# Optimization experiments

Measured on AMD Instinct MI355X. Metric: run time of the kernel, lower is better.

The kernel has to match this reference:

```python
import jax, jax.numpy as jnp
import numpy as np

B, S, H = 16, 2048, 768
MAX_NUM = 400     # max relation pairs per sample (ragged, masked)
LABELS = 97
MID = 768


def setup_inputs() -> dict:
    key = jax.random.key(0)
    k1, k2, k3, k4, k5 = jax.random.split(key, 5)
    outs = jax.random.normal(k1, (B, S, H), dtype=jnp.float32)
    rels = jax.random.randint(k2, (B, MAX_NUM), 0, LABELS)
    start = jnp.ones((B,), dtype=jnp.int32)                     # markers start at pos 1
    num = jax.random.randint(k3, (B,), 1, MAX_NUM + 1)          # ragged counts in [1, MAX_NUM]
    rels_pos = jnp.stack([start, num], axis=1)                  # [B, 2]
    W1 = jax.random.normal(k4, (2 * H, MID), dtype=jnp.float32) * (1.0 / np.sqrt(2 * H))
    b1 = jnp.zeros((MID,), dtype=jnp.float32)
    W2 = jax.random.normal(k5, (MID, LABELS), dtype=jnp.float32) * (1.0 / np.sqrt(MID))
    b2 = jnp.zeros((LABELS,), dtype=jnp.float32)
    return {"outs": outs, "rels": rels, "rels_pos": rels_pos,
            "W1": W1, "b1": b1, "W2": W2, "b2": b2}


def reference(outs, rels, rels_pos, W1, b1, W2, b2):
    # outs: [B, S, H] encoder hidden states; rels_pos[:, 0]=start, [:, 1]=num (ragged)
    start = rels_pos[:, 0]          # [B]
    num = rels_pos[:, 1]            # [B]
    i = jnp.arange(MAX_NUM)         # [N]
    mask = i[None, :] < num[:, None]                 # [B, N] valid-pair mask
    pos1 = start[:, None] + 4 * i[None, :]           # head marker positions
    pos2 = pos1 + 2                                  # tail marker positions
    pos1 = jnp.clip(pos1, 0, S - 1)
    pos2 = jnp.clip(pos2, 0, S - 1)
    v1 = jnp.take_along_axis(outs, pos1[:, :, None], axis=1)   # [B, N, H]
    v2 = jnp.take_along_axis(outs, pos2[:, :, None], axis=1)   # [B, N, H]
    marker_vec = jnp.concatenate([v1, v2], axis=-1)             # [B, N, 2H]
    h = jax.nn.relu(jnp.einsum('bnd,dm->bnm', marker_vec, W1) + b1)
    logits = jnp.einsum('bnm,ml->bnl', h, W2) + b2              # [B, N, L]
    logp = jax.nn.log_softmax(logits, axis=-1)
    nll = -jnp.take_along_axis(logp, rels[:, :, None], axis=-1)[..., 0]  # [B, N]
    maskf = mask.astype(logits.dtype)
    loss = jnp.sum(nll * maskf) / jnp.sum(maskf)                # mean CE over valid pairs
    pred = jnp.where(mask, jnp.argmax(logits, axis=-1), -1)     # [B, N], -1 = padding
    label_vec = jnp.where(mask, rels, -1)
    return loss, pred, label_vec
```

## Files before the change

### kernel.cpp

```cpp
#include <hip/hip_runtime.h>
#include <hip/hip_bf16.h>
#include <math.h>

#define BB   16
#define SS   2048
#define HH   768
#define MAXN 400
#define LBL  97
#define MIDD 768
#define KTOT 1536

#define K2_XTILES 25
#define W1S_JOBS  (192 * 768)

typedef __attribute__((ext_vector_type(8)))  __bf16 bf16x8;
typedef __attribute__((ext_vector_type(16))) float  f32x16;

__global__ __launch_bounds__(256)
void k0_split(const float* __restrict__ W1, ushort* __restrict__ hi,
              ushort* __restrict__ lo)
{
    const int job = blockIdx.x * 256 + threadIdx.x;
    if (job >= W1S_JOBS) return;
    const int g   = job / 768;
    const int col = job - g * 768;
    bf16x8 hv, lv;
    #pragma unroll
    for (int j = 0; j < 8; ++j) {
        const float f = W1[(size_t)(g * 8 + j) * MIDD + col];
        const __bf16 hb = (__bf16)f;
        hv[j] = hb;
        lv[j] = (__bf16)(f - (float)hb);
    }
    ((bf16x8*)hi)[job] = hv;
    ((bf16x8*)lo)[job] = lv;
}

__global__ __launch_bounds__(256, 4)
void k1_gemm1(const float* __restrict__ outs, const int* __restrict__ rels_pos,
              const ushort* __restrict__ w1hi, const ushort* __restrict__ w1lo,
              const float* __restrict__ b1, float* __restrict__ h)
{
    const int b  = blockIdx.z;
    const int n0 = blockIdx.x * 128;
    const int i0 = blockIdx.y * 64;
    const int num = rels_pos[2 * b + 1];
    if (i0 >= num) return;
    const int start = rels_pos[2 * b + 0];

    __shared__ __bf16 Ah[4][64][8];
    __shared__ __bf16 Al[4][64][8];
    __shared__ __bf16 Bh[4][128][8];
    __shared__ __bf16 Bl[4][128][8];

    const int tid = threadIdx.x;

    const int srow = tid & 63;
    const int sg   = tid >> 6;
    const int irow = i0 + srow;
    int p1 = start + 4 * irow;     p1 = min(max(p1, 0), SS - 1);
    int p2 = start + 4 * irow + 2; p2 = min(max(p2, 0), SS - 1);
    const float* arow1 = outs + (size_t)(b * SS + p1) * HH;
    const float* arow2 = outs + (size_t)(b * SS + p2) * HH;

    const int bc  = tid & 127;
    const int bg1 = tid >> 7;
    const int bg2 = 2 + (tid >> 7);
    const bf16x8* WH = (const bf16x8*)w1hi;
    const bf16x8* WL = (const bf16x8*)w1lo;

    const int lane = tid & 63;
    const int wid  = tid >> 6;
    const int wr   = wid >> 1;
    const int wc   = wid & 1;
    const int l31  = lane & 31;
    const int lhi  = lane >> 5;

    f32x16 acc[2];
    #pragma unroll
    for (int n = 0; n < 2; ++n)
        #pragma unroll
        for (int j = 0; j < 16; ++j) acc[n][j] = 0.f;

    float4 aU, aV;
    bf16x8 pB0, pB1, pB2, pB3;
    {
        const int k = sg * 8;
        const float* s = arow1 + k;
        aU = *(const float4*)(s);
        aV = *(const float4*)(s + 4);
        const size_t i1 = (size_t)bg1 * 768 + n0 + bc;
        const size_t i2 = (size_t)bg2 * 768 + n0 + bc;
        pB0 = WH[i1]; pB1 = WL[i1]; pB2 = WH[i2]; pB3 = WL[i2];
    }

    for (int kt = 0; kt < KTOT / 32; ++kt) {
        {
            const float fa[8] = {aU.x, aU.y, aU.z, aU.w, aV.x, aV.y, aV.z, aV.w};
            bf16x8 ah, al;
            #pragma unroll
            for (int j = 0; j < 8; ++j) {
                const __bf16 hb = (__bf16)fa[j];
                ah[j] = hb;
                al[j] = (__bf16)(fa[j] - (float)hb);
            }
            *(bf16x8*)&Ah[sg][srow][0] = ah;
            *(bf16x8*)&Al[sg][srow][0] = al;
            *(bf16x8*)&Bh[bg1][bc][0]  = pB0;
            *(bf16x8*)&Bl[bg1][bc][0]  = pB1;
            *(bf16x8*)&Bh[bg2][bc][0]  = pB2;
            *(bf16x8*)&Bl[bg2][bc][0]  = pB3;
        }
        __syncthreads();

        if (kt + 1 < KTOT / 32) {
            const int k0 = (kt + 1) * 32;
            const int k  = k0 + sg * 8;
            const float* s = (k < HH) ? (arow1 + k) : (arow2 + (k - HH));
            aU = *(const float4*)(s);
            aV = *(const float4*)(s + 4);
            const size_t base = (size_t)(k0 >> 3) * 768 + n0 + bc;
            const size_t i1 = base + (size_t)bg1 * 768;
            const size_t i2 = base + (size_t)bg2 * 768;
            pB0 = WH[i1]; pB1 = WL[i1]; pB2 = WH[i2]; pB3 = WL[i2];
        }

        #pragma unroll
        for (int s = 0; s < 2; ++s) {
            const int kg   = 2 * s + lhi;
            const int arow = wr * 32 + l31;
            const bf16x8 xh = *(const bf16x8*)&Ah[kg][arow][0];
            const bf16x8 xl = *(const bf16x8*)&Al[kg][arow][0];
            #pragma unroll
            for (int n = 0; n < 2; ++n) {
                const int bcol = wc * 64 + n * 32 + l31;
                const bf16x8 yh = *(const bf16x8*)&Bh[kg][bcol][0];
                const bf16x8 yl = *(const bf16x8*)&Bl[kg][bcol][0];
                acc[n] = __builtin_amdgcn_mfma_f32_32x32x16_bf16(xh, yh, acc[n], 0, 0, 0);
                acc[n] = __builtin_amdgcn_mfma_f32_32x32x16_bf16(xh, yl, acc[n], 0, 0, 0);
                acc[n] = __builtin_amdgcn_mfma_f32_32x32x16_bf16(xl, yh, acc[n], 0, 0, 0);
            }
        }
        __syncthreads();
    }

    #pragma unroll
    for (int n = 0; n < 2; ++n) {
        const int colg = n0 + wc * 64 + n * 32 + l31;
        const float bv = b1[colg];
        #pragma unroll
        for (int j = 0; j < 16; ++j) {
            const int row = (j & 3) + 8 * (j >> 2) + 4 * lhi;
            const int i = i0 + wr * 32 + row;
            if (i < MAXN)
                h[((size_t)b * MAXN + i) * MIDD + colg] = fmaxf(acc[n][j] + bv, 0.f);
        }
    }
}

__global__ __launch_bounds__(256, 2)
void k2_head(const float* __restrict__ h, const int* __restrict__ rels,
             const int* __restrict__ rels_pos,
             const float* __restrict__ W2, const float* __restrict__ b2,
             float* __restrict__ out, float* __restrict__ partials)
{
    const int b   = blockIdx.y;
    const int i0  = blockIdx.x * 16;
    const int num = rels_pos[2 * b + 1];
    const int tid = threadIdx.x;
    const int blk = blockIdx.y * gridDim.x + blockIdx.x;

    if (tid < 16) {
        const int i = i0 + tid;
        if (i < MAXN && i >= num) {
            out[1 + b * MAXN + i] = -1.0f;
            out[1 + BB * MAXN + b * MAXN + i] = -1.0f;
        }
    }
    if (i0 >= num) { if (tid == 0) partials[blk] = 0.f; return; }

    __shared__ __align__(16) float hs[MIDD][16];
    __shared__ float wave_nll[4];

    {
        const int row = tid & 15;
        const int kc0 = (tid >> 4) * 4;
        const int hrow_i = min(i0 + row, MAXN - 1);
        const float* hrow = h + ((size_t)b * MAXN + hrow_i) * MIDD;
        #pragma unroll
        for (int j = 0; j < 12; ++j) {
            const int k = kc0 + j * 64;
            const float4 v = *(const float4*)(hrow + k);
            hs[k + 0][row] = v.x;
            hs[k + 1][row] = v.y;
            hs[k + 2][row] = v.z;
            hs[k + 3][row] = v.w;
        }
    }
    __syncthreads();

    const int lane = tid & 63;
    const int wv   = tid >> 6;
    const int c    = lane;
    const bool has2 = (lane + 64) < LBL;
    const int c2   = has2 ? (lane + 64) : (LBL - 1);

    float acc0[4], acc1[4];
    #pragma unroll
    for (int r = 0; r < 4; ++r) { acc0[r] = 0.f; acc1[r] = 0.f; }

    float wA[8], wB[8], nAr[8], nBr[8];
    #pragma unroll
    for (int j = 0; j < 8; ++j) {
        wA[j] = W2[(size_t)j * LBL + c];
        wB[j] = W2[(size_t)j * LBL + c2];
    }
    for (int kbase = 0; kbase < MIDD; kbase += 8) {
        const bool more = (kbase + 8) < MIDD;
        if (more) {
            #pragma unroll
            for (int j = 0; j < 8; ++j) {
                nAr[j] = W2[(size_t)(kbase + 8 + j) * LBL + c];
                nBr[j] = W2[(size_t)(kbase + 8 + j) * LBL + c2];
            }
        }
        #pragma unroll
        for (int j = 0; j < 8; ++j) {
            const float4 hv = *(const float4*)&hs[kbase + j][wv * 4];
            acc0[0] += hv.x * wA[j]; acc0[1] += hv.y * wA[j];
            acc0[2] += hv.z * wA[j]; acc0[3] += hv.w * wA[j];
            acc1[0] += hv.x * wB[j]; acc1[1] += hv.y * wB[j];
            acc1[2] += hv.z * wB[j]; acc1[3] += hv.w * wB[j];
        }
        if (more) {
            #pragma unroll
            for (int j = 0; j < 8; ++j) { wA[j] = nAr[j]; wB[j] = nBr[j]; }
        }
    }
    const float bc  = b2[c];
    const float bc2 = b2[c2];
    #pragma unroll
    for (int r = 0; r < 4; ++r) { acc0[r] += bc; acc1[r] += bc2; }

    float nll_acc = 0.f;
    #pragma unroll
    for (int r = 0; r < 4; ++r) {
        const int i = i0 + wv * 4 + r;
        if (i >= num || i >= MAXN) continue;
        const float v1 = acc0[r];
        const float v2 = has2 ? acc1[r] : -INFINITY;
        float bv = v1; int bi = c;
        if (v2 > v1) { bv = v2; bi = lane + 64; }
        #pragma unroll
        for (int off = 32; off > 0; off >>= 1) {
            const float ov = __shfl_xor(bv, off);
            const int   oi = __shfl_xor(bi, off);
            if (ov > bv || (ov == bv && oi < bi)) { bv = ov; bi = oi; }
        }
        float se = expf(v1 - bv) + (has2 ? expf(v2 - bv) : 0.f);
        #pragma unroll
        for (int off = 32; off > 0; off >>= 1) se += __shfl_xor(se, off);
        const int lbl = rels[b * MAXN + i];
        float tv = (c == lbl ? v1 : 0.f) + ((has2 && (lane + 64) == lbl) ? v2 : 0.f);
        #pragma unroll
        for (int off = 32; off > 0; off >>= 1) tv += __shfl_xor(tv, off);
        const float nll = bv + logf(se) - tv;
        if (lane == 0) {
            nll_acc += nll;
            out[1 + b * MAXN + i] = (float)bi;
            out[1 + BB * MAXN + b * MAXN + i] = (float)lbl;
        }
    }
    if (lane == 0) wave_nll[wv] = nll_acc;
    __syncthreads();
    if (tid == 0)
        partials[blk] = wave_nll[0] + wave_nll[1] + wave_nll[2] + wave_nll[3];
}

__global__ void k3_final(const float* __restrict__ partials,
                         const int* __restrict__ rels_pos, float* __restrict__ out)
{
    const int lane = threadIdx.x;
    float v = 0.f;
    for (int idx = lane; idx < K2_XTILES * BB; idx += 64) v += partials[idx];
    #pragma unroll
    for (int off = 32; off > 0; off >>= 1) v += __shfl_xor(v, off);
    float cnt = (lane < BB) ? (float)min(max(rels_pos[2 * lane + 1], 0), MAXN) : 0.f;
    #pragma unroll
    for (int off = 32; off > 0; off >>= 1) cnt += __shfl_xor(cnt, off);
    if (lane == 0) out[0] = v / cnt;
}

extern "C" void kernel_launch(void* const* d_in, const int* in_sizes, int n_in,
                              void* d_out, int out_size, void* d_ws, size_t ws_size,
                              hipStream_t stream)
{
    const float* outs     = (const float*)d_in[0];
    const int*   rels     = (const int*)  d_in[1];
    const int*   rels_pos = (const int*)  d_in[2];
    const float* W1       = (const float*)d_in[3];
    const float* b1       = (const float*)d_in[4];
    const float* W2       = (const float*)d_in[5];
    const float* b2       = (const float*)d_in[6];
    float* out = (float*)d_out;

    float*  h        = (float*)d_ws;
    float*  partials = h + (size_t)BB * MAXN * MIDD;
    ushort* w1hi     = (ushort*)(partials + K2_XTILES * BB);
    ushort* w1lo     = w1hi + (size_t)W1S_JOBS * 8;

    hipLaunchKernelGGL(k0_split, dim3((W1S_JOBS + 255) / 256), dim3(256), 0, stream,
                       W1, w1hi, w1lo);

    dim3 g1(MIDD / 128, (MAXN + 63) / 64, BB);
    hipLaunchKernelGGL(k1_gemm1, g1, dim3(256), 0, stream,
                       outs, rels_pos, w1hi, w1lo, b1, h);

    dim3 g2(K2_XTILES, BB);
    hipLaunchKernelGGL(k2_head, g2, dim3(256), 0, stream,
                       h, rels, rels_pos, W2, b2, out, partials);

    hipLaunchKernelGGL(k3_final, dim3(1), dim3(64), 0, stream, partials, rels_pos, out);
}
```

Baseline: 298.4 us.

## Deepen GEMM1 register prefetch to two stages and remap blocks to a 1D grid

The GEMM1 kernel now keeps two sets of prefetch registers so global loads run two K-tiles ahead of the MFMA work, which is meant to hide more global-memory latency. The 3D grid becomes a 1D grid with a swizzled index that places the 8 consecutive blocks of a group on different (batch,row-tile) groups sharing the same column tile, which may improve W1 reuse in L2 or spread blocks across XCDs. Launch bounds drop from 4 to 2 waves per SIMD to leave room for the extra registers, which reduces occupancy.

```diff
diff --git a/kernel.cpp b/kernel.cpp
--- a/kernel.cpp
+++ b/kernel.cpp
@@ -12,6 +12,9 @@
 
 #define K2_XTILES 25
 #define W1S_JOBS  (192 * 768)
+#define K1_RT     7
+#define K1_GROUPS (K1_RT * BB)
+#define K1_BLOCKS (K1_GROUPS * 6)
 
 typedef __attribute__((ext_vector_type(8)))  __bf16 bf16x8;
 typedef __attribute__((ext_vector_type(16))) float  f32x16;
@@ -36,14 +39,20 @@
     ((bf16x8*)lo)[job] = lv;
 }
 
-__global__ __launch_bounds__(256, 4)
+__global__ __launch_bounds__(256, 2)
 void k1_gemm1(const float* __restrict__ outs, const int* __restrict__ rels_pos,
               const ushort* __restrict__ w1hi, const ushort* __restrict__ w1lo,
               const float* __restrict__ b1, float* __restrict__ h)
 {
-    const int b  = blockIdx.z;
-    const int n0 = blockIdx.x * 128;
-    const int i0 = blockIdx.y * 64;
+    const int gid = blockIdx.x;
+    const int idx = gid >> 3;
+    const int g   = (gid & 7) + 8 * (idx / 6);
+    const int m   = idx % 6;
+    const int rt  = g % K1_RT;
+    const int b   = g / K1_RT;
+    const int n0  = m * 128;
+    const int i0  = rt * 64;
+
     const int num = rels_pos[2 * b + 1];
     if (i0 >= num) return;
     const int start = rels_pos[2 * b + 0];
@@ -82,67 +91,94 @@
         #pragma unroll
         for (int j = 0; j < 16; ++j) acc[n][j] = 0.f;
 
-    float4 aU, aV;
-    bf16x8 pB0, pB1, pB2, pB3;
+    float4 aU0, aV0, aU1, aV1;
+    bf16x8 pB00, pB01, pB02, pB03, pB10, pB11, pB12, pB13;
+
     {
         const int k = sg * 8;
         const float* s = arow1 + k;
-        aU = *(const float4*)(s);
-        aV = *(const float4*)(s + 4);
+        aU0 = *(const float4*)(s);
+        aV0 = *(const float4*)(s + 4);
         const size_t i1 = (size_t)bg1 * 768 + n0 + bc;
         const size_t i2 = (size_t)bg2 * 768 + n0 + bc;
-        pB0 = WH[i1]; pB1 = WL[i1]; pB2 = WH[i2]; pB3 = WL[i2];
-    }
-
-    for (int kt = 0; kt < KTOT / 32; ++kt) {
-        {
-            const float fa[8] = {aU.x, aU.y, aU.z, aU.w, aV.x, aV.y, aV.z, aV.w};
-            bf16x8 ah, al;
-            #pragma unroll
-            for (int j = 0; j < 8; ++j) {
-                const __bf16 hb = (__bf16)fa[j];
-                ah[j] = hb;
-                al[j] = (__bf16)(fa[j] - (float)hb);
-            }
-            *(bf16x8*)&Ah[sg][srow][0] = ah;
-            *(bf16x8*)&Al[sg][srow][0] = al;
-            *(bf16x8*)&Bh[bg1][bc][0]  = pB0;
-            *(bf16x8*)&Bl[bg1][bc][0]  = pB1;
-            *(bf16x8*)&Bh[bg2][bc][0]  = pB2;
-            *(bf16x8*)&Bl[bg2][bc][0]  = pB3;
-        }
+        pB00 = WH[i1]; pB01 = WL[i1]; pB02 = WH[i2]; pB03 = WL[i2];
+    }
+    {
+        const int k = 32 + sg * 8;
+        const float* s = arow1 + k;
+        aU1 = *(const float4*)(s);
+        aV1 = *(const float4*)(s + 4);
+        const size_t base = (size_t)(32 >> 3) * 768 + n0 + bc;
+        const size_t i1 = base + (size_t)bg1 * 768;
+        const size_t i2 = base + (size_t)bg2 * 768;
+        pB10 = WH[i1]; pB11 = WL[i1]; pB12 = WH[i2]; pB13 = WL[i2];
+    }
+
+    #define K1_STAGE(AU, AV, P0, P1_, P2_, P3_)                               \
+        {                                                                     \
+            const float fa[8] = {AU.x, AU.y, AU.z, AU.w,                      \
+                                 AV.x, AV.y, AV.z, AV.w};                     \
+            bf16x8 ah, al;                                                    \
+            _Pragma("unroll")                                                 \
+            for (int j = 0; j < 8; ++j) {                                     \
+                const __bf16 hb = (__bf16)fa[j];                              \
+                ah[j] = hb;                                                   \
+                al[j] = (__bf16)(fa[j] - (float)hb);                          \
+            }                                                                 \
+            *(bf16x8*)&Ah[sg][srow][0] = ah;                                  \
+            *(bf16x8*)&Al[sg][srow][0] = al;                                  \
+            *(bf16x8*)&Bh[bg1][bc][0]  = P0;                                  \
+            *(bf16x8*)&Bl[bg1][bc][0]  = P1_;                                 \
+            *(bf16x8*)&Bh[bg2][bc][0]  = P2_;                                 \
+            *(bf16x8*)&Bl[bg2][bc][0]  = P3_;                                 \
+        }
+
+    #define K1_LOAD(AU, AV, P0, P1_, P2_, P3_, KT)                            \
+        {                                                                     \
+            const int k0 = (KT) * 32;                                         \
+            const int k  = k0 + sg * 8;                                       \
+            const float* s = (k < HH) ? (arow1 + k) : (arow2 + (k - HH));     \
+            AU = *(const float4*)(s);                                         \
+            AV = *(const float4*)(s + 4);                                     \
+            const size_t base = (size_t)(k0 >> 3) * 768 + n0 + bc;            \
+            const size_t i1 = base + (size_t)bg1 * 768;                       \
+            const size_t i2 = base + (size_t)bg2 * 768;                       \
+            P0 = WH[i1]; P1_ = WL[i1]; P2_ = WH[i2]; P3_ = WL[i2];            \
+        }
+
+    #define K1_MFMA()                                                         \
+        _Pragma("unroll")                                                     \
+        for (int s = 0; s < 2; ++s) {                                         \
+            const int kg   = 2 * s + lhi;                                     \
+            const int arow = wr * 32 + l31;                                   \
+            const bf16x8 xh = *(const bf16x8*)&Ah[kg][arow][0];               \
+            const bf16x8 xl = *(const bf16x8*)&Al[kg][arow][0];               \
+            _Pragma("unroll")                                                 \
+            for (int n = 0; n < 2; ++n) {                                     \
+                const int bcol = wc * 64 + n * 32 + l31;                      \
+                const bf16x8 yh = *(const bf16x8*)&Bh[kg][bcol][0];           \
+                const bf16x8 yl = *(const bf16x8*)&Bl[kg][bcol][0];           \
+                acc[n] = __builtin_amdgcn_mfma_f32_32x32x16_bf16(xh, yh, acc[n], 0, 0, 0); \
+                acc[n] = __builtin_amdgcn_mfma_f32_32x32x16_bf16(xh, yl, acc[n], 0, 0, 0); \
+                acc[n] = __builtin_amdgcn_mfma_f32_32x32x16_bf16(xl, yh, acc[n], 0, 0, 0); \
+            }                                                                 \
+        }
+
+    for (int kt = 0; kt < KTOT / 32; kt += 2) {
+        K1_STAGE(aU0, aV0, pB00, pB01, pB02, pB03);
         __syncthreads();
-
-        if (kt + 1 < KTOT / 32) {
-            const int k0 = (kt + 1) * 32;
-            const int k  = k0 + sg * 8;
-            const float* s = (k < HH) ? (arow1 + k) : (arow2 + (k - HH));
-            aU = *(const float4*)(s);
-            aV = *(const float4*)(s + 4);
-            const size_t base = (size_t)(k0 >> 3) * 768 + n0 + bc;
-            const size_t i1 = base + (size_t)bg1 * 768;
-            const size_t i2 = base + (size_t)bg2 * 768;
-            pB0 = WH[i1]; pB1 = WL[i1]; pB2 = WH[i2]; pB3 = WL[i2];
-        }
-
-        #pragma unroll
-        for (int s = 0; s < 2; ++s) {
-            const int kg   = 2 * s + lhi;
-            const int arow = wr * 32 + l31;
-            const bf16x8 xh = *(const bf16x8*)&Ah[kg][arow][0];
-            const bf16x8 xl = *(const bf16x8*)&Al[kg][arow][0];
-            #pragma unroll
-            for (int n = 0; n < 2; ++n) {
-                const int bcol = wc * 64 + n * 32 + l31;
-                const bf16x8 yh = *(const bf16x8*)&Bh[kg][bcol][0];
-                const bf16x8 yl = *(const bf16x8*)&Bl[kg][bcol][0];
-                acc[n] = __builtin_amdgcn_mfma_f32_32x32x16_bf16(xh, yh, acc[n], 0, 0, 0);
-                acc[n] = __builtin_amdgcn_mfma_f32_32x32x16_bf16(xh, yl, acc[n], 0, 0, 0);
-                acc[n] = __builtin_amdgcn_mfma_f32_32x32x16_bf16(xl, yh, acc[n], 0, 0, 0);
-            }
-        }
+        if (kt + 2 < KTOT / 32) K1_LOAD(aU0, aV0, pB00, pB01, pB02, pB03, kt + 2);
+        K1_MFMA();
         __syncthreads();
-    }
+        K1_STAGE(aU1, aV1, pB10, pB11, pB12, pB13);
+        __syncthreads();
+        if (kt + 3 < KTOT / 32) K1_LOAD(aU1, aV1, pB10, pB11, pB12, pB13, kt + 3);
+        K1_MFMA();
+        __syncthreads();
+    }
+    #undef K1_STAGE
+    #undef K1_LOAD
+    #undef K1_MFMA
 
     #pragma unroll
     for (int n = 0; n < 2; ++n) {
@@ -312,8 +348,7 @@
     hipLaunchKernelGGL(k0_split, dim3((W1S_JOBS + 255) / 256), dim3(256), 0, stream,
                        W1, w1hi, w1lo);
 
-    dim3 g1(MIDD / 128, (MAXN + 63) / 64, BB);
-    hipLaunchKernelGGL(k1_gemm1, g1, dim3(256), 0, stream,
+    hipLaunchKernelGGL(k1_gemm1, dim3(K1_BLOCKS), dim3(256), 0, stream,
                        outs, rels_pos, w1hi, w1lo, b1, h);
 
     dim3 g2(K2_XTILES, BB);
```

Result: faster. 287.3 us (-3.7%).
